# Performance work log

Hardware: AMD Instinct MI355X
Metric: run time of the kernel (lower is better)

Reference implementation:

```python
import jax, jax.numpy as jnp
import numpy as np

B, T, H, N = 4, 2048, 1024, 16
DT_MIN, DT_MAX = 1e-3, 1e-1
A_INIT_MIN, A_INIT_MAX = 0.5, 2.0


def _inv_softplus(x):
    # log(exp(x) - 1), numerically stable
    return x + jnp.log(-jnp.expm1(-x))


def setup_inputs() -> dict:
    key = jax.random.key(0)
    kx, ka, kb, kc, kw, kdt = jax.random.split(key, 6)
    x = jax.random.normal(kx, (B, T, H), dtype=jnp.float32)
    A_log = jax.random.uniform(ka, (H, N), minval=np.log(A_INIT_MIN), maxval=np.log(A_INIT_MAX), dtype=jnp.float32)
    B_mat = 0.02 * jax.random.normal(kb, (H, N), dtype=jnp.float32)
    C_mat = 0.02 * jax.random.normal(kc, (H, N), dtype=jnp.float32)
    D_vec = jnp.ones((H,), dtype=jnp.float32)
    W_dt = 0.02 * jax.random.normal(kw, (H, H), dtype=jnp.float32)
    b_dt = _inv_softplus(jax.random.uniform(kdt, (H,), minval=DT_MIN, maxval=DT_MAX, dtype=jnp.float32))
    return {"x": x, "A_log": A_log, "B_mat": B_mat, "C_mat": C_mat, "D_vec": D_vec, "W_dt": W_dt, "b_dt": b_dt}


def reference(x, A_log, B_mat, C_mat, D_vec, W_dt, b_dt):
    # in_proj is Identity since input_size == hidden_size
    u = x  # (B, T, H)
    A = -jnp.exp(A_log)  # (H, N)
    # dt for all timesteps at once: softplus(u @ W_dt^T + b_dt) -> (B, T, H)
    dt = jax.nn.softplus(jnp.einsum('bth,gh->btg', u, W_dt) + b_dt)
    state0 = jnp.zeros((u.shape[0], A_log.shape[0], A_log.shape[1]), dtype=u.dtype)

    def step(state, inp):
        dt_t, u_t = inp  # (B, H), (B, H)
        dtA = dt_t[..., None]  # (B, H, 1)
        A_bar = jnp.exp(dtA * A)                       # (B, H, N)
        state = A_bar * state + (dtA * B_mat) * u_t[..., None]
        y_t = jnp.einsum('bhn,hn->bh', state, C_mat) + D_vec * u_t
        return state, y_t

    # scan over time axis
    state_final, ys = jax.lax.scan(step, state0, (dt.transpose(1, 0, 2), u.transpose(1, 0, 2)))
    out = ys.transpose(1, 0, 2)  # (B, T, H)
    return out, state_final
```

## Files before the change

### kernel.cpp

```cpp
#include <hip/hip_runtime.h>
#include <stdint.h>

#define BB 4
#define TT 2048
#define HH 1024
#define NN 16
#define KK 1024
#define GG 1024
#define MM (BB*TT)
#define NCHUNK 128
#define TC (TT/NCHUNK)
#define HB 256

#if __has_builtin(__builtin_amdgcn_exp2f)
#define FAST_EXP2(x) __builtin_amdgcn_exp2f(x)
#else
#define FAST_EXP2(x) __expf((x) * 0.6931471805599453f)
#endif
#define EXPSCALE 1.4426950408889634f

typedef __attribute__((ext_vector_type(8))) short short8;
typedef __attribute__((ext_vector_type(4))) float f32x4;

__device__ __forceinline__ unsigned short f2bf(float f) {
  union { float f; unsigned u; } a; a.f = f;
  unsigned u = a.u;
  u += 0x7fffu + ((u >> 16) & 1u);
  return (unsigned short)(u >> 16);
}

__device__ __forceinline__ unsigned pack_half2(float a, float b) {
  union { _Float16 h[2]; unsigned u; } p;
  p.h[0] = (_Float16)a; p.h[1] = (_Float16)b;
  return p.u;
}

__global__ __launch_bounds__(256) void cvt2_f32_bf16(const float* __restrict__ srcA,
                                                     unsigned short* __restrict__ dstA, int n4a,
                                                     const float* __restrict__ srcB,
                                                     unsigned short* __restrict__ dstB, int n4b) {
  int i = blockIdx.x * blockDim.x + threadIdx.x;
  const float* s; unsigned short* d; int j;
  if (i < n4a) { s = srcA; d = dstA; j = i; }
  else         { s = srcB; d = dstB; j = i - n4a; if (j >= n4b) return; }
  float4 a = ((const float4*)s)[j];
  ushort4 o;
  o.x = f2bf(a.x); o.y = f2bf(a.y); o.z = f2bf(a.z); o.w = f2bf(a.w);
  ((ushort4*)d)[j] = o;
}

__global__ __launch_bounds__(256, 4) void gemm_dt(const unsigned short* __restrict__ xb,
                                                  const unsigned short* __restrict__ wb,
                                                  const float* __restrict__ b_dt,
                                                  _Float16* __restrict__ dtH) {
  __shared__ short lsA[128 * 64];
  __shared__ short lsB[64 * 64];
  const int tid  = threadIdx.x;
  const int w    = tid >> 6;
  const int lane = tid & 63;
  const int bid  = blockIdx.x;
  const int swz  = (bid & 7) * 128 + (bid >> 3);
  const int m0 = (swz >> 4) * 128;
  const int g0 = (swz & 15) * 64;

  const int r8 = lane >> 3;
  const int c8 = (lane & 7) * 8;
  const unsigned short* gA[4];
  short*                lA[4];
#pragma unroll
  for (int q = 0; q < 4; ++q) {
    const int row = w * 32 + q * 8 + r8;
    gA[q] = xb + (size_t)(m0 + row) * KK + c8;
    lA[q] = lsA + row * 64;
  }
  const unsigned short* gB[2];
  short*                lB[2];
#pragma unroll
  for (int q = 0; q < 2; ++q) {
    const int row = w * 16 + q * 8 + r8;
    gB[q] = wb + (size_t)(g0 + row) * KK + c8;
    lB[q] = lsB + row * 64;
  }

  const int wm   = (w >> 1) * 64;
  const int wg   = (w & 1) * 32;
  const int lrow = lane & 15;
  const int lq   = lane >> 4;

  int aoff[4][2], boff[2][2];
#pragma unroll
  for (int mi = 0; mi < 4; ++mi) {
    const int row = wm + mi * 16 + lrow;
    aoff[mi][0] = row * 64 + lq * 8;
    aoff[mi][1] = row * 64 + 32 + lq * 8;
  }
#pragma unroll
  for (int ni = 0; ni < 2; ++ni) {
    const int row = wg + ni * 16 + lrow;
    boff[ni][0] = row * 64 + lq * 8;
    boff[ni][1] = row * 64 + 32 + lq * 8;
  }

  f32x4 acc[4][2];
  const f32x4 zero = {0.f, 0.f, 0.f, 0.f};
#pragma unroll
  for (int i = 0; i < 4; ++i)
#pragma unroll
    for (int j = 0; j < 2; ++j) acc[i][j] = zero;

  for (int kt = 0; kt < KK / 64; ++kt) {
    const int ko = kt * 64;
#pragma unroll
    for (int q = 0; q < 4; ++q)
      __builtin_amdgcn_global_load_lds((__attribute__((address_space(1))) void*)(gA[q] + ko),
                                       (__attribute__((address_space(3))) void*)(lA[q]), 16, 0, 0);
#pragma unroll
    for (int q = 0; q < 2; ++q)
      __builtin_amdgcn_global_load_lds((__attribute__((address_space(1))) void*)(gB[q] + ko),
                                       (__attribute__((address_space(3))) void*)(lB[q]), 16, 0, 0);
    __syncthreads();

#pragma unroll
    for (int kk = 0; kk < 2; ++kk) {
      short8 af[4], bfr[2];
#pragma unroll
      for (int mi = 0; mi < 4; ++mi) af[mi] = *(const short8*)&lsA[aoff[mi][kk]];
#pragma unroll
      for (int ni = 0; ni < 2; ++ni) bfr[ni] = *(const short8*)&lsB[boff[ni][kk]];
#pragma unroll
      for (int mi = 0; mi < 4; ++mi)
#pragma unroll
        for (int ni = 0; ni < 2; ++ni)
          acc[mi][ni] = __builtin_amdgcn_mfma_f32_16x16x32_bf16(af[mi], bfr[ni], acc[mi][ni], 0, 0, 0);
    }
    __syncthreads();
  }

  const int mrow = m0 + wm + lq * 4;
#pragma unroll
  for (int ni = 0; ni < 2; ++ni) {
    const int g = g0 + wg + ni * 16 + lrow;
    const float bias = b_dt[g];
#pragma unroll
    for (int mi = 0; mi < 4; ++mi)
#pragma unroll
      for (int r = 0; r < 4; ++r) {
        float z = acc[mi][ni][r] + bias;
        dtH[(size_t)(mrow + mi * 16 + r) * GG + g] =
            (_Float16)(fmaxf(z, 0.f) + __logf(1.f + __expf(-fabsf(z))));
      }
  }
}

__device__ __forceinline__ void p1_load8(const float* __restrict__ up,
                                         const _Float16* __restrict__ dp, int t0,
                                         float (&U)[8], _Float16 (&D)[8]) {
#pragma unroll
  for (int i = 0; i < 8; ++i) {
    U[i] = up[(size_t)(t0 + i) * HH];
    D[i] = dp[(size_t)(t0 + i) * HH];
  }
}

__device__ __forceinline__ void p1_comp8(const float (&U)[8], const _Float16 (&D)[8], int t0,
                                         float (&s)[NN], float& sd,
                                         const float (&Ae)[NN], const float (&Cb)[NN],
                                         float Dv, unsigned* __restrict__ yp) {
#pragma unroll
  for (int i = 0; i < 8; ++i) {
    const float dtv = (float)D[i];
    const float uv  = U[i];
    const float du  = dtv * uv;
    sd += dtv;
    float y0 = Dv * uv, y1 = 0.f, y2 = 0.f, y3 = 0.f;
#pragma unroll
    for (int n = 0; n < NN; n += 4) {
      float ab;
      ab = FAST_EXP2(dtv * Ae[n]);     s[n]     = fmaf(ab, s[n],     du); y0 = fmaf(Cb[n],     s[n],     y0);
      ab = FAST_EXP2(dtv * Ae[n + 1]); s[n + 1] = fmaf(ab, s[n + 1], du); y1 = fmaf(Cb[n + 1], s[n + 1], y1);
      ab = FAST_EXP2(dtv * Ae[n + 2]); s[n + 2] = fmaf(ab, s[n + 2], du); y2 = fmaf(Cb[n + 2], s[n + 2], y2);
      ab = FAST_EXP2(dtv * Ae[n + 3]); s[n + 3] = fmaf(ab, s[n + 3], du); y3 = fmaf(Cb[n + 3], s[n + 3], y3);
    }
    yp[(size_t)(t0 + i) * HH] = pack_half2((y0 + y1) + (y2 + y3), sd);
  }
}

__global__ __launch_bounds__(256, 4) void ssm_phase1(const float* __restrict__ x,
                                                     const _Float16* __restrict__ dtH,
                                                     const float* __restrict__ A_log,
                                                     const float* __restrict__ Bm_,
                                                     const float* __restrict__ Cm_,
                                                     const float* __restrict__ Dv_,
                                                     float* __restrict__ sloc,
                                                     float* __restrict__ sdArr,
                                                     unsigned* __restrict__ ylsd) {
  const int tid = threadIdx.x;
  const int bid = blockIdx.x;
  const int hb = bid & (HH / HB - 1);
  const int b  = (bid >> 2) & (BB - 1);
  const int c  = bid >> 4;
  const int h  = hb * HB + tid;

  const size_t base = ((size_t)b * TT + c * TC) * HH + h;
  const float*    up = x + base;
  const _Float16* dp = dtH + base;
  unsigned*       yp = ylsd + base;

  float Ae[NN], Cb[NN];
#pragma unroll
  for (int n = 0; n < NN; n += 4) {
    f32x4 av = *(const f32x4*)&A_log[h * NN + n];
    f32x4 cv = *(const f32x4*)&Cm_[h * NN + n];
    f32x4 bv = *(const f32x4*)&Bm_[h * NN + n];
#pragma unroll
    for (int q = 0; q < 4; ++q) {
      Ae[n + q] = -__expf(av[q]) * EXPSCALE;
      Cb[n + q] = cv[q] * bv[q];
    }
  }
  const float Dv = Dv_[h];

  float s[NN];
#pragma unroll
  for (int n = 0; n < NN; ++n) s[n] = 0.f;
  float sd = 0.f;

  float Ua[8], Ub[8];
  _Float16 Da[8], Db[8];
  p1_load8(up, dp, 0, Ua, Da);
  p1_load8(up, dp, 8, Ub, Db);
  p1_comp8(Ua, Da, 0, s, sd, Ae, Cb, Dv, yp);
  p1_comp8(Ub, Db, 8, s, sd, Ae, Cb, Dv, yp);

  float* sp = sloc + (((size_t)c * BB + b) * HH + h) * NN;
#pragma unroll
  for (int n = 0; n < NN; n += 4) {
    f32x4 v = {s[n], s[n + 1], s[n + 2], s[n + 3]};
    *(f32x4*)&sp[n] = v;
  }
  sdArr[((size_t)c * BB + b) * HH + h] = sd;
}

__global__ __launch_bounds__(256) void ssm_phase2(float* __restrict__ sloc,
                                                  const float* __restrict__ sdArr,
                                                  const float* __restrict__ A_log,
                                                  const float* __restrict__ Bm_,
                                                  float* __restrict__ stateOut) {
  const int id = blockIdx.x * 256 + threadIdx.x;
  const int hn = id & (HH * NN - 1);
  const int bh = id >> 4;
  const float Ae = -__expf(A_log[hn]) * EXPSCALE;
  float carry = 0.f;
#pragma unroll 4
  for (int ch = 0; ch < NCHUNK; ++ch) {
    const size_t idx = (size_t)ch * (BB * HH * NN) + id;
    const float sl = sloc[idx];
    const float dc = FAST_EXP2(Ae * sdArr[(size_t)ch * (BB * HH) + bh]);
    sloc[idx] = carry;
    carry = fmaf(dc, carry, sl);
  }
  stateOut[id] = Bm_[hn] * carry;
}

__device__ __forceinline__ void p3_load8(const unsigned* __restrict__ yp, int t0,
                                         unsigned (&V)[8]) {
#pragma unroll
  for (int i = 0; i < 8; ++i) V[i] = yp[(size_t)(t0 + i) * HH];
}

__device__ __forceinline__ void p3_comp8(const unsigned (&V)[8], int t0,
                                         const float (&Ae)[NN], const float (&cc)[NN],
                                         float* __restrict__ yo) {
#pragma unroll
  for (int i = 0; i < 8; ++i) {
    union { unsigned u; _Float16 hh[2]; } q; q.u = V[i];
    const float sdv = (float)q.hh[1];
    float y0 = (float)q.hh[0], y1 = 0.f, y2 = 0.f, y3 = 0.f;
#pragma unroll
    for (int n = 0; n < NN; n += 4) {
      y0 = fmaf(cc[n],     FAST_EXP2(Ae[n]     * sdv), y0);
      y1 = fmaf(cc[n + 1], FAST_EXP2(Ae[n + 1] * sdv), y1);
      y2 = fmaf(cc[n + 2], FAST_EXP2(Ae[n + 2] * sdv), y2);
      y3 = fmaf(cc[n + 3], FAST_EXP2(Ae[n + 3] * sdv), y3);
    }
    yo[(size_t)(t0 + i) * HH] = (y0 + y1) + (y2 + y3);
  }
}

__global__ __launch_bounds__(256, 4) void ssm_phase3(const unsigned* __restrict__ ylsd,
                                                     const float* __restrict__ A_log,
                                                     const float* __restrict__ Bm_,
                                                     const float* __restrict__ Cm_,
                                                     const float* __restrict__ carryBuf,
                                                     float* __restrict__ out) {
  const int tid = threadIdx.x;
  const int bid = blockIdx.x;
  const int hb = bid & (HH / HB - 1);
  const int b  = (bid >> 2) & (BB - 1);
  const int c  = bid >> 4;
  const int h  = hb * HB + tid;

  const size_t base = ((size_t)b * TT + c * TC) * HH + h;
  const unsigned* yp = ylsd + base;
  float*          yo = out + base;

  float Ae[NN], cc[NN];
  const float* cp = carryBuf + (((size_t)c * BB + b) * HH + h) * NN;
#pragma unroll
  for (int n = 0; n < NN; n += 4) {
    f32x4 av = *(const f32x4*)&A_log[h * NN + n];
    f32x4 cv = *(const f32x4*)&Cm_[h * NN + n];
    f32x4 bv = *(const f32x4*)&Bm_[h * NN + n];
    f32x4 kv = *(const f32x4*)&cp[n];
#pragma unroll
    for (int q = 0; q < 4; ++q) {
      Ae[n + q] = -__expf(av[q]) * EXPSCALE;
      cc[n + q] = cv[q] * bv[q] * kv[q];
    }
  }

  unsigned Va[8], Vb[8];
  p3_load8(yp, 0, Va);
  p3_load8(yp, 8, Vb);
  p3_comp8(Va, 0, Ae, cc, yo);
  p3_comp8(Vb, 8, Ae, cc, yo);
}

extern "C" void kernel_launch(void* const* d_in, const int* in_sizes, int n_in,
                              void* d_out, int out_size, void* d_ws, size_t ws_size,
                              hipStream_t stream) {
  const float* x     = (const float*)d_in[0];
  const float* A_log = (const float*)d_in[1];
  const float* B_mat = (const float*)d_in[2];
  const float* C_mat = (const float*)d_in[3];
  const float* D_vec = (const float*)d_in[4];
  const float* W_dt  = (const float*)d_in[5];
  const float* b_dt  = (const float*)d_in[6];
  float* out = (float*)d_out;

  char* ws = (char*)d_ws;
  unsigned short* xb   = (unsigned short*)(ws);
  unsigned short* wb   = (unsigned short*)(ws + 16777216);
  _Float16*       dtH  = (_Float16*)(ws + 18874368);
  unsigned*       ylsd = (unsigned*)(ws + 35651584);
  float*          sloc  = (float*)(ws + 69206016);
  float*          sdArr = (float*)(ws + 102760448);
  float* stateOut = out + (size_t)BB * TT * HH;

  const int n4x = MM * KK / 4, n4w = GG * KK / 4;
  cvt2_f32_bf16<<<(n4x + n4w + 255) / 256, 256, 0, stream>>>(x, xb, n4x, W_dt, wb, n4w);
  gemm_dt<<<(MM / 128) * (GG / 64), 256, 0, stream>>>(xb, wb, b_dt, dtH);

  const int nblk = (HH / HB) * BB * NCHUNK;
  ssm_phase1<<<nblk, 256, 0, stream>>>(x, dtH, A_log, B_mat, C_mat, D_vec, sloc, sdArr, ylsd);
  ssm_phase2<<<(BB * HH * NN) / 256, 256, 0, stream>>>(sloc, sdArr, A_log, B_mat, stateOut);
  ssm_phase3<<<nblk, 256, 0, stream>>>(ylsd, A_log, B_mat, C_mat, sloc, out);
}
```

Measured before the change: 207.7 us.

## Recompute chunk scan in phase 3 from carried state instead of correction terms

```diff
diff --git a/kernel.cpp b/kernel.cpp
--- a/kernel.cpp
+++ b/kernel.cpp
@@ -8,7 +8,7 @@
 #define KK 1024
 #define GG 1024
 #define MM (BB*TT)
-#define NCHUNK 128
+#define NCHUNK 64
 #define TC (TT/NCHUNK)
 #define HB 256
 
@@ -27,12 +27,6 @@
   unsigned u = a.u;
   u += 0x7fffu + ((u >> 16) & 1u);
   return (unsigned short)(u >> 16);
-}
-
-__device__ __forceinline__ unsigned pack_half2(float a, float b) {
-  union { _Float16 h[2]; unsigned u; } p;
-  p.h[0] = (_Float16)a; p.h[1] = (_Float16)b;
-  return p.u;
 }
 
 __global__ __launch_bounds__(256) void cvt2_f32_bf16(const float* __restrict__ srcA,
@@ -152,48 +146,11 @@
   }
 }
 
-__device__ __forceinline__ void p1_load8(const float* __restrict__ up,
-                                         const _Float16* __restrict__ dp, int t0,
-                                         float (&U)[8], _Float16 (&D)[8]) {
-#pragma unroll
-  for (int i = 0; i < 8; ++i) {
-    U[i] = up[(size_t)(t0 + i) * HH];
-    D[i] = dp[(size_t)(t0 + i) * HH];
-  }
-}
-
-__device__ __forceinline__ void p1_comp8(const float (&U)[8], const _Float16 (&D)[8], int t0,
-                                         float (&s)[NN], float& sd,
-                                         const float (&Ae)[NN], const float (&Cb)[NN],
-                                         float Dv, unsigned* __restrict__ yp) {
-#pragma unroll
-  for (int i = 0; i < 8; ++i) {
-    const float dtv = (float)D[i];
-    const float uv  = U[i];
-    const float du  = dtv * uv;
-    sd += dtv;
-    float y0 = Dv * uv, y1 = 0.f, y2 = 0.f, y3 = 0.f;
-#pragma unroll
-    for (int n = 0; n < NN; n += 4) {
-      float ab;
-      ab = FAST_EXP2(dtv * Ae[n]);     s[n]     = fmaf(ab, s[n],     du); y0 = fmaf(Cb[n],     s[n],     y0);
-      ab = FAST_EXP2(dtv * Ae[n + 1]); s[n + 1] = fmaf(ab, s[n + 1], du); y1 = fmaf(Cb[n + 1], s[n + 1], y1);
-      ab = FAST_EXP2(dtv * Ae[n + 2]); s[n + 2] = fmaf(ab, s[n + 2], du); y2 = fmaf(Cb[n + 2], s[n + 2], y2);
-      ab = FAST_EXP2(dtv * Ae[n + 3]); s[n + 3] = fmaf(ab, s[n + 3], du); y3 = fmaf(Cb[n + 3], s[n + 3], y3);
-    }
-    yp[(size_t)(t0 + i) * HH] = pack_half2((y0 + y1) + (y2 + y3), sd);
-  }
-}
-
 __global__ __launch_bounds__(256, 4) void ssm_phase1(const float* __restrict__ x,
                                                      const _Float16* __restrict__ dtH,
                                                      const float* __restrict__ A_log,
-                                                     const float* __restrict__ Bm_,
-                                                     const float* __restrict__ Cm_,
-                                                     const float* __restrict__ Dv_,
                                                      float* __restrict__ sloc,
-                                                     float* __restrict__ sdArr,
-                                                     unsigned* __restrict__ ylsd) {
+                                                     float* __restrict__ sdArr) {
   const int tid = threadIdx.x;
   const int bid = blockIdx.x;
   const int hb = bid & (HH / HB - 1);
@@ -204,33 +161,40 @@
   const size_t base = ((size_t)b * TT + c * TC) * HH + h;
   const float*    up = x + base;
   const _Float16* dp = dtH + base;
-  unsigned*       yp = ylsd + base;
-
-  float Ae[NN], Cb[NN];
+
+  float Ae[NN];
 #pragma unroll
   for (int n = 0; n < NN; n += 4) {
     f32x4 av = *(const f32x4*)&A_log[h * NN + n];
-    f32x4 cv = *(const f32x4*)&Cm_[h * NN + n];
-    f32x4 bv = *(const f32x4*)&Bm_[h * NN + n];
-#pragma unroll
-    for (int q = 0; q < 4; ++q) {
-      Ae[n + q] = -__expf(av[q]) * EXPSCALE;
-      Cb[n + q] = cv[q] * bv[q];
-    }
-  }
-  const float Dv = Dv_[h];
+#pragma unroll
+    for (int q = 0; q < 4; ++q) Ae[n + q] = -__expf(av[q]) * EXPSCALE;
+  }
 
   float s[NN];
 #pragma unroll
   for (int n = 0; n < NN; ++n) s[n] = 0.f;
   float sd = 0.f;
 
-  float Ua[8], Ub[8];
-  _Float16 Da[8], Db[8];
-  p1_load8(up, dp, 0, Ua, Da);
-  p1_load8(up, dp, 8, Ub, Db);
-  p1_comp8(Ua, Da, 0, s, sd, Ae, Cb, Dv, yp);
-  p1_comp8(Ub, Db, 8, s, sd, Ae, Cb, Dv, yp);
+#pragma unroll
+  for (int j = 0; j < TC / 8; ++j) {
+    float uu[8], dv[8];
+#pragma unroll
+    for (int i = 0; i < 8; ++i) {
+      uu[i] = up[(size_t)(j * 8 + i) * HH];
+      dv[i] = (float)dp[(size_t)(j * 8 + i) * HH];
+    }
+#pragma unroll
+    for (int i = 0; i < 8; ++i) {
+      const float dtv = dv[i];
+      const float du  = dtv * uu[i];
+      sd += dtv;
+#pragma unroll
+      for (int n = 0; n < NN; ++n) {
+        const float ab = FAST_EXP2(dtv * Ae[n]);
+        s[n] = fmaf(ab, s[n], du);
+      }
+    }
+  }
 
   float* sp = sloc + (((size_t)c * BB + b) * HH + h) * NN;
 #pragma unroll
@@ -251,7 +215,7 @@
   const int bh = id >> 4;
   const float Ae = -__expf(A_log[hn]) * EXPSCALE;
   float carry = 0.f;
-#pragma unroll 4
+#pragma unroll 8
   for (int ch = 0; ch < NCHUNK; ++ch) {
     const size_t idx = (size_t)ch * (BB * HH * NN) + id;
     const float sl = sloc[idx];
@@ -262,35 +226,12 @@
   stateOut[id] = Bm_[hn] * carry;
 }
 
-__device__ __forceinline__ void p3_load8(const unsigned* __restrict__ yp, int t0,
-                                         unsigned (&V)[8]) {
-#pragma unroll
-  for (int i = 0; i < 8; ++i) V[i] = yp[(size_t)(t0 + i) * HH];
-}
-
-__device__ __forceinline__ void p3_comp8(const unsigned (&V)[8], int t0,
-                                         const float (&Ae)[NN], const float (&cc)[NN],
-                                         float* __restrict__ yo) {
-#pragma unroll
-  for (int i = 0; i < 8; ++i) {
-    union { unsigned u; _Float16 hh[2]; } q; q.u = V[i];
-    const float sdv = (float)q.hh[1];
-    float y0 = (float)q.hh[0], y1 = 0.f, y2 = 0.f, y3 = 0.f;
-#pragma unroll
-    for (int n = 0; n < NN; n += 4) {
-      y0 = fmaf(cc[n],     FAST_EXP2(Ae[n]     * sdv), y0);
-      y1 = fmaf(cc[n + 1], FAST_EXP2(Ae[n + 1] * sdv), y1);
-      y2 = fmaf(cc[n + 2], FAST_EXP2(Ae[n + 2] * sdv), y2);
-      y3 = fmaf(cc[n + 3], FAST_EXP2(Ae[n + 3] * sdv), y3);
-    }
-    yo[(size_t)(t0 + i) * HH] = (y0 + y1) + (y2 + y3);
-  }
-}
-
-__global__ __launch_bounds__(256, 4) void ssm_phase3(const unsigned* __restrict__ ylsd,
+__global__ __launch_bounds__(256, 4) void ssm_phase3(const float* __restrict__ x,
+                                                     const _Float16* __restrict__ dtH,
                                                      const float* __restrict__ A_log,
                                                      const float* __restrict__ Bm_,
                                                      const float* __restrict__ Cm_,
+                                                     const float* __restrict__ Dv_,
                                                      const float* __restrict__ carryBuf,
                                                      float* __restrict__ out) {
   const int tid = threadIdx.x;
@@ -301,29 +242,57 @@
   const int h  = hb * HB + tid;
 
   const size_t base = ((size_t)b * TT + c * TC) * HH + h;
-  const unsigned* yp = ylsd + base;
+  const float*    up = x + base;
+  const _Float16* dp = dtH + base;
   float*          yo = out + base;
 
-  float Ae[NN], cc[NN];
-  const float* cp = carryBuf + (((size_t)c * BB + b) * HH + h) * NN;
+  float Ae[NN], Cb[NN];
 #pragma unroll
   for (int n = 0; n < NN; n += 4) {
     f32x4 av = *(const f32x4*)&A_log[h * NN + n];
     f32x4 cv = *(const f32x4*)&Cm_[h * NN + n];
     f32x4 bv = *(const f32x4*)&Bm_[h * NN + n];
-    f32x4 kv = *(const f32x4*)&cp[n];
 #pragma unroll
     for (int q = 0; q < 4; ++q) {
       Ae[n + q] = -__expf(av[q]) * EXPSCALE;
-      cc[n + q] = cv[q] * bv[q] * kv[q];
-    }
-  }
-
-  unsigned Va[8], Vb[8];
-  p3_load8(yp, 0, Va);
-  p3_load8(yp, 8, Vb);
-  p3_comp8(Va, 0, Ae, cc, yo);
-  p3_comp8(Vb, 8, Ae, cc, yo);
+      Cb[n + q] = cv[q] * bv[q];
+    }
+  }
+  const float Dv = Dv_[h];
+
+  float s[NN];
+  const float* cp = carryBuf + (((size_t)c * BB + b) * HH + h) * NN;
+#pragma unroll
+  for (int n = 0; n < NN; n += 4) {
+    f32x4 v = *(const f32x4*)&cp[n];
+    s[n] = v[0]; s[n + 1] = v[1]; s[n + 2] = v[2]; s[n + 3] = v[3];
+  }
+
+#pragma unroll
+  for (int j = 0; j < TC / 8; ++j) {
+    float uu[8], dv[8];
+#pragma unroll
+    for (int i = 0; i < 8; ++i) {
+      uu[i] = up[(size_t)(j * 8 + i) * HH];
+      dv[i] = (float)dp[(size_t)(j * 8 + i) * HH];
+    }
+#pragma unroll
+    for (int i = 0; i < 8; ++i) {
+      const float dtv = dv[i];
+      const float uv  = uu[i];
+      const float du  = dtv * uv;
+      float y0 = Dv * uv, y1 = 0.f, y2 = 0.f, y3 = 0.f;
+#pragma unroll
+      for (int n = 0; n < NN; n += 4) {
+        float ab;
+        ab = FAST_EXP2(dtv * Ae[n]);     s[n]     = fmaf(ab, s[n],     du); y0 = fmaf(Cb[n],     s[n],     y0);
+        ab = FAST_EXP2(dtv * Ae[n + 1]); s[n + 1] = fmaf(ab, s[n + 1], du); y1 = fmaf(Cb[n + 1], s[n + 1], y1);
+        ab = FAST_EXP2(dtv * Ae[n + 2]); s[n + 2] = fmaf(ab, s[n + 2], du); y2 = fmaf(Cb[n + 2], s[n + 2], y2);
+        ab = FAST_EXP2(dtv * Ae[n + 3]); s[n + 3] = fmaf(ab, s[n + 3], du); y3 = fmaf(Cb[n + 3], s[n + 3], y3);
+      }
+      yo[(size_t)(j * 8 + i) * HH] = (y0 + y1) + (y2 + y3);
+    }
+  }
 }
 
 extern "C" void kernel_launch(void* const* d_in, const int* in_sizes, int n_in,
@@ -342,9 +311,8 @@
   unsigned short* xb   = (unsigned short*)(ws);
   unsigned short* wb   = (unsigned short*)(ws + 16777216);
   _Float16*       dtH  = (_Float16*)(ws + 18874368);
-  unsigned*       ylsd = (unsigned*)(ws + 35651584);
-  float*          sloc  = (float*)(ws + 69206016);
-  float*          sdArr = (float*)(ws + 102760448);
+  float*          sloc  = (float*)(ws);
+  float*          sdArr = (float*)(ws + 16777216);
   float* stateOut = out + (size_t)BB * TT * HH;
 
   const int n4x = MM * KK / 4, n4w = GG * KK / 4;
@@ -352,7 +320,7 @@
   gemm_dt<<<(MM / 128) * (GG / 64), 256, 0, stream>>>(xb, wb, b_dt, dtH);
 
   const int nblk = (HH / HB) * BB * NCHUNK;
-  ssm_phase1<<<nblk, 256, 0, stream>>>(x, dtH, A_log, B_mat, C_mat, D_vec, sloc, sdArr, ylsd);
+  ssm_phase1<<<nblk, 256, 0, stream>>>(x, dtH, A_log, sloc, sdArr);
   ssm_phase2<<<(BB * HH * NN) / 256, 256, 0, stream>>>(sloc, sdArr, A_log, B_mat, stateOut);
-  ssm_phase3<<<nblk, 256, 0, stream>>>(ylsd, A_log, B_mat, C_mat, sloc, out);
-}
+  ssm_phase3<<<nblk, 256, 0, stream>>>(x, dtH, A_log, B_mat, C_mat, D_vec, sloc, out);
+}
```

After: 180.4 us. 13.2% less time.
